# Optimization experiments

Hardware: AMD Instinct MI355X
Metric: run time of the kernel (lower is better)

Reference implementation:

```python
import jax, jax.numpy as jnp
import numpy as np

B, M, C, S, SD, K, H = 32, 448, 384, 512, 128, 8, 8
DH = C // H
EPS = 1e-5
NEG_SLOPE = 0.2


def setup_inputs() -> dict:
    key = jax.random.key(0)
    ks = iter(jax.random.split(key, 32))
    nrm = lambda shape, scale=0.05: (jax.random.normal(next(ks), shape, jnp.float32) * scale)
    inp = {
        'q': jax.random.normal(next(ks), (B, M, C), jnp.float32),
        'coarse': jax.random.normal(next(ks), (B, M, 3), jnp.float32),
        'skeleton': jax.random.normal(next(ks), (B, S, 3), jnp.float32),
        # GraphConv 1: 3 -> 64 (root weight, rel/neighbor weight, bias)
        'gc1_wroot': nrm((3, 64), 0.3), 'gc1_wrel': nrm((3, 64), 0.3), 'gc1_b': jnp.zeros((64,), jnp.float32),
        # GraphConv 2: 64 -> SD
        'gc2_wroot': nrm((64, SD), 0.1), 'gc2_wrel': nrm((64, SD), 0.1), 'gc2_b': jnp.zeros((SD,), jnp.float32),
        # skeleton_projection: SD -> C
        'proj_w': nrm((SD, C), 0.08), 'proj_b': jnp.zeros((C,), jnp.float32),
        # MultiheadAttention (torch layout: in_proj (3C, C), out_proj (C, C))
        'attn_in_w': nrm((3 * C, C), 0.05), 'attn_in_b': jnp.zeros((3 * C,), jnp.float32),
        'attn_out_w': nrm((C, C), 0.05), 'attn_out_b': jnp.zeros((C,), jnp.float32),
        # increase_dim: Conv1d(C,1024,1) + BN(1024) + LeakyReLU + Conv1d(1024,1024,1)
        'inc1_w': nrm((1024, C), 0.05), 'inc1_b': jnp.zeros((1024,), jnp.float32),
        'bn_g': jnp.ones((1024,), jnp.float32), 'bn_b': jnp.zeros((1024,), jnp.float32),
        'bn_m': jnp.zeros((1024,), jnp.float32), 'bn_v': jnp.ones((1024,), jnp.float32),
        'inc2_w': nrm((1024, 1024), 0.03), 'inc2_b': jnp.zeros((1024,), jnp.float32),
        # reduce_map: Linear(C + 1024 + 3, C)
        'red_w': nrm((1024 + C + 3, C), 0.03), 'red_b': jnp.zeros((C,), jnp.float32),
    }
    return inp


def _knn_idx(pts):
    # pts: [B,S,3]; per-batch kNN (self excluded), matching knn_graph(k=K, batch=...)
    d2 = jnp.sum((pts[:, :, None, :] - pts[:, None, :, :]) ** 2, axis=-1)  # [B,S,S]
    d2 = d2 + jnp.eye(S, dtype=pts.dtype)[None] * 1e10                       # mask self
    _, idx = jax.lax.top_k(-d2, K)                                           # [B,S,K]
    return idx


def _graph_conv(x, idx, wroot, wrel, b):
    # GraphConv (PyG, aggr='add'): out_i = x_i Wroot + (sum_{j in N(i)} x_j) Wrel + b
    nb = jax.vmap(lambda f, i: f[i])(x, idx)   # [B,S,K,F]
    agg = nb.sum(axis=2)                       # [B,S,F]
    return x @ wroot + agg @ wrel + b


def reference(q, coarse, skeleton, gc1_wroot, gc1_wrel, gc1_b, gc2_wroot, gc2_wrel, gc2_b,
              proj_w, proj_b, attn_in_w, attn_in_b, attn_out_w, attn_out_b,
              inc1_w, inc1_b, bn_g, bn_b, bn_m, bn_v, inc2_w, inc2_b, red_w, red_b):
    # --- skeleton branch: knn graph + 2-layer GraphConv + max-pool + projection ---
    idx = _knn_idx(skeleton)
    h = _graph_conv(skeleton, idx, gc1_wroot, gc1_wrel, gc1_b)
    h = jax.nn.relu(h)
    h = _graph_conv(h, idx, gc2_wroot, gc2_wrel, gc2_b)        # [B,S,SD]
    proxy = jnp.max(h, axis=1)                                  # [B,SD]
    proxy = proxy @ proj_w + proj_b                             # [B,C]
    kv = jnp.broadcast_to(proxy[:, None, :], (B, M, C))         # expanded proxies

    # --- cross attention (torch nn.MultiheadAttention math) ---
    wq, wk, wv = attn_in_w[:C], attn_in_w[C:2 * C], attn_in_w[2 * C:]
    bq, bk, bv = attn_in_b[:C], attn_in_b[C:2 * C], attn_in_b[2 * C:]
    qh = (q @ wq.T + bq).reshape(B, M, H, DH)
    kh = (kv @ wk.T + bk).reshape(B, M, H, DH)
    vh = (kv @ wv.T + bv).reshape(B, M, H, DH)
    scores = jnp.einsum('bmhd,bnhd->bhmn', qh, kh) / jnp.sqrt(jnp.float32(DH))
    attn = jax.nn.softmax(scores, axis=-1)
    ctx = jnp.einsum('bhmn,bnhd->bmhd', attn, vh).reshape(B, M, C)
    q = ctx @ attn_out_w.T + attn_out_b                         # fused features [B,M,C]

    # --- increase_dim (1x1 conv == matmul) + BN(eval) + LeakyReLU + 1x1 conv ---
    g = jnp.einsum('bmc,oc->bmo', q, inc1_w) + inc1_b           # [B,M,1024]
    g = bn_g * (g - bn_m) * jax.lax.rsqrt(bn_v + EPS) + bn_b
    g = jnp.where(g >= 0, g, NEG_SLOPE * g)
    g = jnp.einsum('bmc,oc->bmo', g, inc2_w) + inc2_b
    global_feature = jnp.max(g, axis=1)                         # [B,1024]

    # --- concat + reduce_map ---
    rebuild = jnp.concatenate([jnp.broadcast_to(global_feature[:, None, :], (B, M, 1024)), q, coarse], axis=-1)
    out = rebuild @ red_w + red_b                               # [B,M,C]
    return out
```

## Files before the change

kernel.cpp:

```cpp
#include <hip/hip_runtime.h>

#define NB 32
#define MM 448
#define CC 384
#define SS 512
#define KNN 8

#define WS_IDX   0u
#define WS_H1    524288u
#define WS_PMAX  (WS_H1 + 4194304u)
#define WS_Q     (WS_PMAX + 262144u)
#define WS_Y     (WS_Q + 49152u)
#define WS_G2    (WS_Y + 131072u)
#define WS_BASEP (WS_G2 + 131072u)
#define WS_PP    WS_H1
#define WS_KV    WS_IDX
#define WS_VV    (WS_IDX + 49152u)

__device__ __forceinline__ float wave_sum(float v) {
#pragma unroll
  for (int m = 1; m < 64; m <<= 1) v += __shfl_xor(v, m, 64);
  return v;
}

__global__ __launch_bounds__(256) void k_knn_gc1(
    const float* __restrict__ skel,
    const float* __restrict__ w1root, const float* __restrict__ w1rel,
    const float* __restrict__ b1,
    int* __restrict__ idx_ws, float* __restrict__ h1_ws)
{
  int b   = blockIdx.x >> 7;
  int grp = blockIdx.x & 127;
  __shared__ __align__(16) float4 sk[SS];
  const float* sb = skel + b * SS * 3;
  for (int t = threadIdx.x; t < SS; t += 256)
    sk[t] = make_float4(sb[t*3+0], sb[t*3+1], sb[t*3+2], 0.f);
  __syncthreads();

  int wave = threadIdx.x >> 6, lane = threadIdx.x & 63;
  int i = grp * 4 + wave;
  float4 pi = sk[i];

  float bd[KNN];
#pragma unroll
  for (int t = 0; t < KNN; t++) {
    int j = lane + (t << 6);
    float4 p = sk[j];
    float d2;
    {
#pragma clang fp contract(off)
      float dx = pi.x - p.x, dy = pi.y - p.y, dz = pi.z - p.z;
      d2 = (dx*dx + dy*dy) + dz*dz;
    }
    bd[t] = (j == i) ? 3e38f : d2;
  }

  int win[KNN];
  int* idx_base = idx_ws + (size_t)(b*SS + i) * KNN;
#pragma unroll
  for (int t = 0; t < KNN; t++) {
    float bestd = bd[0]; int bests = 0;
#pragma unroll
    for (int s = 1; s < KNN; s++)
      if (bd[s] < bestd) { bestd = bd[s]; bests = s; }
    int bestj = lane + (bests << 6);
#pragma unroll
    for (int m = 1; m < 64; m <<= 1) {
      float od = __shfl_xor(bestd, m, 64);
      int   oj = __shfl_xor(bestj, m, 64);
      if (od < bestd || (od == bestd && oj < bestj)) { bestd = od; bestj = oj; }
    }
    win[t] = bestj;
    if (lane == t) idx_base[t] = bestj;
    if ((bestj & 63) == lane) {
      int sl = bestj >> 6;
#pragma unroll
      for (int s = 0; s < KNN; s++) if (s == sl) bd[s] = 3e38f;
    }
  }

  float a0 = 0.f, a1 = 0.f, a2 = 0.f;
#pragma unroll
  for (int t = 0; t < KNN; t++) {
    float4 n = sk[win[t]];
    a0 += n.x; a1 += n.y; a2 += n.z;
  }

  int c = lane;
  float h = b1[c] + pi.x*w1root[c] + pi.y*w1root[64+c] + pi.z*w1root[128+c]
                  + a0*w1rel[c]   + a1*w1rel[64+c]   + a2*w1rel[128+c];
  h = fmaxf(h, 0.f);
  h1_ws[(size_t)(b*SS + i) * 64 + lane] = h;
}

__global__ __launch_bounds__(256) void k_gc2_max(
    const float* __restrict__ h1_ws, const int* __restrict__ idx_ws,
    const float* __restrict__ w2root, const float* __restrict__ w2rel,
    const float* __restrict__ b2, float* __restrict__ pmax)
{
  int b = blockIdx.x >> 4, chunk = blockIdx.x & 15;
  int r0 = chunk * 32;
  __shared__ __align__(16) float X[32*129];
  __shared__ __align__(16) float Wt[32*128];
  __shared__ float mred[8*128];
  __shared__ int nbs[32*KNN];

  const float* h1b = h1_ws + (size_t)b * SS * 64;
  nbs[threadIdx.x] = idx_ws[(b*SS + r0)*KNN + threadIdx.x];
#pragma unroll
  for (int p = 0; p < 8; p++) {
    int idx = threadIdx.x + 256*p;
    int r = idx >> 6, k = idx & 63;
    X[r*129 + k] = h1b[(r0 + r)*64 + k];
  }
  __syncthreads();
#pragma unroll
  for (int p = 0; p < 8; p++) {
    int idx = threadIdx.x + 256*p;
    int r = idx >> 6, k = idx & 63;
    const int* nb = nbs + r*KNN;
    float s = 0.f;
#pragma unroll
    for (int j = 0; j < KNN; j++) s += h1b[nb[j]*64 + k];
    X[r*129 + 64 + k] = s;
  }

  int rg = threadIdx.x >> 5, cg = threadIdx.x & 31;
  float acc[4][4];
#pragma unroll
  for (int r = 0; r < 4; r++)
#pragma unroll
    for (int u = 0; u < 4; u++) acc[r][u] = 0.f;

  const float* wsrc[4] = { w2root, w2root + 32*128, w2rel, w2rel + 32*128 };
#pragma unroll 1
  for (int ch = 0; ch < 4; ch++) {
    __syncthreads();
    const float* ws = wsrc[ch];
#pragma unroll
    for (int p = 0; p < 16; p++) {
      int idx = threadIdx.x + 256*p;
      Wt[idx] = ws[idx];
    }
    __syncthreads();
    int kb = ch * 32;
    const float* xr0 = X + (rg*4+0)*129 + kb;
    const float* xr1 = X + (rg*4+1)*129 + kb;
    const float* xr2 = X + (rg*4+2)*129 + kb;
    const float* xr3 = X + (rg*4+3)*129 + kb;
#pragma unroll 4
    for (int k = 0; k < 32; k++) {
      float4 w4 = *(const float4*)(Wt + k*128 + cg*4);
      float x0 = xr0[k], x1 = xr1[k], x2 = xr2[k], x3 = xr3[k];
      acc[0][0] += x0*w4.x; acc[0][1] += x0*w4.y; acc[0][2] += x0*w4.z; acc[0][3] += x0*w4.w;
      acc[1][0] += x1*w4.x; acc[1][1] += x1*w4.y; acc[1][2] += x1*w4.z; acc[1][3] += x1*w4.w;
      acc[2][0] += x2*w4.x; acc[2][1] += x2*w4.y; acc[2][2] += x2*w4.z; acc[2][3] += x2*w4.w;
      acc[3][0] += x3*w4.x; acc[3][1] += x3*w4.y; acc[3][2] += x3*w4.z; acc[3][3] += x3*w4.w;
    }
  }
#pragma unroll
  for (int u = 0; u < 4; u++)
    mred[rg*128 + cg*4 + u] =
      fmaxf(fmaxf(acc[0][u], acc[1][u]), fmaxf(acc[2][u], acc[3][u]));
  __syncthreads();
  if (threadIdx.x < 128) {
    int col = threadIdx.x;
    float mx = mred[col];
#pragma unroll
    for (int g = 1; g < 8; g++) mx = fmaxf(mx, mred[g*128 + col]);
    pmax[(size_t)(b*16 + chunk)*128 + col] = mx + b2[col];
  }
}

__global__ __launch_bounds__(384) void k_proxy_kv(
    const float* __restrict__ pmax,
    const float* __restrict__ proj_w, const float* __restrict__ proj_b,
    float* __restrict__ kv_ws)
{
  int b = blockIdx.x, t = threadIdx.x;
  __shared__ float proxy[128];
  if (t < 128) {
    float m = -3e38f;
    for (int ch = 0; ch < 16; ch++) m = fmaxf(m, pmax[(size_t)(b*16 + ch)*128 + t]);
    proxy[t] = m;
  }
  __syncthreads();
  float acc = proj_b[t];
  for (int s = 0; s < 128; s++) acc += proxy[s] * proj_w[s*CC + t];
  kv_ws[b*CC + t] = acc;
}

__global__ __launch_bounds__(256) void k_mv384(
    const float* __restrict__ xin, const float* __restrict__ w, int row0,
    const float* __restrict__ bias, int bias0, float* __restrict__ out)
{
  int b = blockIdx.x, og = blockIdx.y;
  int wv = threadIdx.x >> 6, lane = threadIdx.x & 63;
  __shared__ float xs[CC];
  for (int t = threadIdx.x; t < CC; t += 256) xs[t] = xin[b*CC + t];
  __syncthreads();
  float x0 = xs[lane*6+0], x1 = xs[lane*6+1], x2 = xs[lane*6+2];
  float x3 = xs[lane*6+3], x4 = xs[lane*6+4], x5 = xs[lane*6+5];
#pragma unroll
  for (int u = 0; u < 8; u++) {
    int o = og*32 + wv*8 + u;
    const float* wr = w + (size_t)(row0 + o) * CC + lane*6;
    float2 wa = *(const float2*)wr;
    float2 wb = *(const float2*)(wr + 2);
    float2 wc = *(const float2*)(wr + 4);
    float p = wa.x*x0 + wa.y*x1 + wb.x*x2 + wb.y*x3 + wc.x*x4 + wc.y*x5;
    p = wave_sum(p);
    if (lane == 0) out[b*CC + o] = bias[bias0 + o] + p;
  }
}

__global__ __launch_bounds__(256) void k_inc1_bn(
    const float* __restrict__ q_ws, const float* __restrict__ inc1_w,
    const float* __restrict__ inc1_b,
    const float* __restrict__ bng, const float* __restrict__ bnb,
    const float* __restrict__ bnm, const float* __restrict__ bnv,
    float* __restrict__ y_ws)
{
  int b = blockIdx.x >> 4, og = blockIdx.x & 15;
  int t = threadIdx.x;
  int o = og*64 + (t >> 2), qq = t & 3;
  __shared__ __align__(16) float xs[CC];
  for (int i = t; i < CC; i += 256) xs[i] = q_ws[b*CC + i];
  __syncthreads();
  const float* wr = inc1_w + (size_t)o * CC + qq*96;
  const float* xr = xs + qq*96;
  float acc = 0.f;
#pragma unroll
  for (int kk = 0; kk < 96; kk += 4) {
    float4 w4 = *(const float4*)(wr + kk);
    float4 x4 = *(const float4*)(xr + kk);
    acc += w4.x*x4.x + w4.y*x4.y + w4.z*x4.z + w4.w*x4.w;
  }
  acc += __shfl_xor(acc, 1, 64);
  acc += __shfl_xor(acc, 2, 64);
  if (qq == 0) {
    float a = acc + inc1_b[o];
    float z = bng[o] * (a - bnm[o]) * rsqrtf(bnv[o] + 1e-5f) + bnb[o];
    y_ws[b*1024 + o] = (z >= 0.f) ? z : 0.2f * z;
  }
}

__global__ __launch_bounds__(256) void k_inc2(
    const float* __restrict__ y_ws, const float* __restrict__ inc2_w,
    const float* __restrict__ inc2_b, float* __restrict__ g2_ws)
{
  int b = blockIdx.x >> 4, og = blockIdx.x & 15;
  int t = threadIdx.x;
  int o = og*64 + (t >> 2), qq = t & 3;
  __shared__ __align__(16) float xs[1024];
  for (int i = t; i < 1024; i += 256) xs[i] = y_ws[b*1024 + i];
  __syncthreads();
  const float* wr = inc2_w + (size_t)o * 1024 + qq*256;
  const float* xr = xs + qq*256;
  float acc = 0.f;
#pragma unroll 8
  for (int kk = 0; kk < 256; kk += 4) {
    float4 w4 = *(const float4*)(wr + kk);
    float4 x4 = *(const float4*)(xr + kk);
    acc += w4.x*x4.x + w4.y*x4.y + w4.z*x4.z + w4.w*x4.w;
  }
  acc += __shfl_xor(acc, 1, 64);
  acc += __shfl_xor(acc, 2, 64);
  if (qq == 0) g2_ws[b*1024 + o] = acc + inc2_b[o];
}

__global__ __launch_bounds__(256) void k_basep(
    const float* __restrict__ g2_ws, const float* __restrict__ q_ws,
    const float* __restrict__ red_w, float* __restrict__ pp)
{
  int cg = blockIdx.x;
  int o0 = blockIdx.y * 64;
  int c0 = cg * 32;
  __shared__ __align__(16) float xs[32*33];
  __shared__ __align__(16) float wt[32*64];
#pragma unroll
  for (int p = 0; p < 8; p++) {
    int idx = threadIdx.x + 256*p;
    int c = idx >> 6, o = idx & 63;
    wt[idx] = red_w[(size_t)(c0 + c)*CC + o0 + o];
  }
  {
    int b = threadIdx.x >> 3, cp = threadIdx.x & 7;
    const float* src = (cg < 32) ? (g2_ws + b*1024 + c0)
                                 : (q_ws  + b*CC   + (c0 - 1024));
    float4 v = *(const float4*)(src + cp*4);
    xs[(cp*4+0)*33 + b] = v.x;
    xs[(cp*4+1)*33 + b] = v.y;
    xs[(cp*4+2)*33 + b] = v.z;
    xs[(cp*4+3)*33 + b] = v.w;
  }
  __syncthreads();
  int b = threadIdx.x >> 3, og = threadIdx.x & 7;
  float acc[8];
#pragma unroll
  for (int u = 0; u < 8; u++) acc[u] = 0.f;
#pragma unroll 8
  for (int c = 0; c < 32; c++) {
    float xv = xs[c*33 + b];
    float4 w0 = *(const float4*)(wt + c*64 + og*8);
    float4 w1 = *(const float4*)(wt + c*64 + og*8 + 4);
    acc[0] += xv*w0.x; acc[1] += xv*w0.y; acc[2] += xv*w0.z; acc[3] += xv*w0.w;
    acc[4] += xv*w1.x; acc[5] += xv*w1.y; acc[6] += xv*w1.z; acc[7] += xv*w1.w;
  }
  float* dst = pp + (size_t)(cg*32 + b)*CC + o0 + og*8;
  *(float4*)dst       = make_float4(acc[0], acc[1], acc[2], acc[3]);
  *(float4*)(dst + 4) = make_float4(acc[4], acc[5], acc[6], acc[7]);
}

__global__ __launch_bounds__(256) void k_base_red(
    const float* __restrict__ pp, float* __restrict__ basep)
{
  int idx = blockIdx.x * 256 + threadIdx.x;
  float s = 0.f;
#pragma unroll 4
  for (int cg = 0; cg < 44; cg++) s += pp[cg*12288 + idx];
  basep[idx] = s;
}

__global__ __launch_bounds__(256) void k_out(
    const float* __restrict__ basep, const float* __restrict__ red_b,
    const float* __restrict__ red_w, const float* __restrict__ coarse,
    float* __restrict__ out)
{
  int gid = blockIdx.x * 256 + threadIdx.x;
  int c4 = gid % 96;
  int row = gid / 96;
  int b = row / 448;
  int c = c4 * 4;
  float4 p0 = *(const float4*)(basep + b*CC + c);
  float4 rb = *(const float4*)(red_b + c);
  const float* cr = coarse + (size_t)row * 3;
  float cx = cr[0], cy = cr[1], cz = cr[2];
  float4 w0 = *(const float4*)(red_w + (size_t)1408*CC + c);
  float4 w1 = *(const float4*)(red_w + (size_t)1409*CC + c);
  float4 w2 = *(const float4*)(red_w + (size_t)1410*CC + c);
  float4 o4;
  o4.x = p0.x + rb.x + cx*w0.x + cy*w1.x + cz*w2.x;
  o4.y = p0.y + rb.y + cx*w0.y + cy*w1.y + cz*w2.y;
  o4.z = p0.z + rb.z + cx*w0.z + cy*w1.z + cz*w2.z;
  o4.w = p0.w + rb.w + cx*w0.w + cy*w1.w + cz*w2.w;
  *(float4*)(out + (size_t)row*CC + c) = o4;
}

extern "C" void kernel_launch(void* const* d_in, const int* in_sizes, int n_in,
                              void* d_out, int out_size, void* d_ws, size_t ws_size,
                              hipStream_t stream)
{
  (void)in_sizes; (void)n_in; (void)out_size; (void)ws_size;
  const float* coarse = (const float*)d_in[1];
  const float* skel   = (const float*)d_in[2];
  const float* g1wr   = (const float*)d_in[3];
  const float* g1wl   = (const float*)d_in[4];
  const float* g1b    = (const float*)d_in[5];
  const float* g2wr   = (const float*)d_in[6];
  const float* g2wl   = (const float*)d_in[7];
  const float* g2b    = (const float*)d_in[8];
  const float* projw  = (const float*)d_in[9];
  const float* projb  = (const float*)d_in[10];
  const float* aiw    = (const float*)d_in[11];
  const float* aib    = (const float*)d_in[12];
  const float* aow    = (const float*)d_in[13];
  const float* aob    = (const float*)d_in[14];
  const float* i1w    = (const float*)d_in[15];
  const float* i1b    = (const float*)d_in[16];
  const float* bng    = (const float*)d_in[17];
  const float* bnb    = (const float*)d_in[18];
  const float* bnm    = (const float*)d_in[19];
  const float* bnv    = (const float*)d_in[20];
  const float* i2w    = (const float*)d_in[21];
  const float* i2b    = (const float*)d_in[22];
  const float* redw   = (const float*)d_in[23];
  const float* redb   = (const float*)d_in[24];
  float* out = (float*)d_out;

  char* ws = (char*)d_ws;
  int*   idx_ws = (int*)(ws + WS_IDX);
  float* h1_ws  = (float*)(ws + WS_H1);
  float* pmax   = (float*)(ws + WS_PMAX);
  float* q_ws   = (float*)(ws + WS_Q);
  float* y_ws   = (float*)(ws + WS_Y);
  float* g2_ws  = (float*)(ws + WS_G2);
  float* basep  = (float*)(ws + WS_BASEP);
  float* pp     = (float*)(ws + WS_PP);
  float* kv_ws  = (float*)(ws + WS_KV);
  float* vv_ws  = (float*)(ws + WS_VV);

  k_knn_gc1<<<4096, 256, 0, stream>>>(skel, g1wr, g1wl, g1b, idx_ws, h1_ws);
  k_gc2_max<<<512, 256, 0, stream>>>(h1_ws, idx_ws, g2wr, g2wl, g2b, pmax);
  k_proxy_kv<<<32, 384, 0, stream>>>(pmax, projw, projb, kv_ws);
  k_mv384<<<dim3(32, 12), 256, 0, stream>>>(kv_ws, aiw, 2*CC, aib, 2*CC, vv_ws);
  k_mv384<<<dim3(32, 12), 256, 0, stream>>>(vv_ws, aow, 0,    aob, 0,    q_ws);
  k_inc1_bn<<<512, 256, 0, stream>>>(q_ws, i1w, i1b, bng, bnb, bnm, bnv, y_ws);
  k_inc2<<<512, 256, 0, stream>>>(y_ws, i2w, i2b, g2_ws);
  k_basep<<<dim3(44, 6), 256, 0, stream>>>(g2_ws, q_ws, redw, pp);
  k_base_red<<<48, 256, 0, stream>>>(pp, basep);
  k_out<<<5376, 256, 0, stream>>>(basep, redb, redw, coarse, out);
}
```

Measured before the change: 234.2 us.

## Fuse all stages into one cooperative persistent kernel with grid syncs

Replaces the ten separate kernel launches with a single cooperative kernel of 512 blocks that runs every stage in turn, separated by grid-wide barriers. Stages that used more blocks now loop over virtual blocks, and smaller stages idle the extra blocks. The goal is to remove per-launch overhead and inter-kernel gaps. In exchange it adds grid.sync costs, lower parallelism for the large kNN and output stages, and a dependence on all 512 blocks being co-resident.

```diff
diff --git a/kernel.cpp b/kernel.cpp
--- a/kernel.cpp
+++ b/kernel.cpp
@@ -1,10 +1,14 @@
 #include <hip/hip_runtime.h>
+#include <hip/hip_cooperative_groups.h>
+
+namespace cg = cooperative_groups;
 
 #define NB 32
 #define MM 448
 #define CC 384
 #define SS 512
 #define KNN 8
+#define NBLK 512
 
 #define WS_IDX   0u
 #define WS_H1    524288u
@@ -17,334 +21,340 @@
 #define WS_KV    WS_IDX
 #define WS_VV    (WS_IDX + 49152u)
 
+struct P {
+  const float *coarse, *skel, *g1wr, *g1wl, *g1b, *g2wr, *g2wl, *g2b,
+              *projw, *projb, *aiw, *aib, *aow, *aob, *i1w, *i1b,
+              *bng, *bnb, *bnm, *bnv, *i2w, *i2b, *redw, *redb;
+  int* idx_ws;
+  float *h1_ws, *pmax, *q_ws, *y_ws, *g2_ws, *basep, *pp, *kv_ws, *vv_ws, *out;
+};
+
 __device__ __forceinline__ float wave_sum(float v) {
 #pragma unroll
   for (int m = 1; m < 64; m <<= 1) v += __shfl_xor(v, m, 64);
   return v;
 }
 
-__global__ __launch_bounds__(256) void k_knn_gc1(
-    const float* __restrict__ skel,
-    const float* __restrict__ w1root, const float* __restrict__ w1rel,
-    const float* __restrict__ b1,
-    int* __restrict__ idx_ws, float* __restrict__ h1_ws)
-{
-  int b   = blockIdx.x >> 7;
-  int grp = blockIdx.x & 127;
-  __shared__ __align__(16) float4 sk[SS];
-  const float* sb = skel + b * SS * 3;
-  for (int t = threadIdx.x; t < SS; t += 256)
-    sk[t] = make_float4(sb[t*3+0], sb[t*3+1], sb[t*3+2], 0.f);
-  __syncthreads();
-
-  int wave = threadIdx.x >> 6, lane = threadIdx.x & 63;
-  int i = grp * 4 + wave;
-  float4 pi = sk[i];
-
-  float bd[KNN];
-#pragma unroll
-  for (int t = 0; t < KNN; t++) {
-    int j = lane + (t << 6);
-    float4 p = sk[j];
-    float d2;
+__global__ __launch_bounds__(256, 2) void k_all(P p) {
+  cg::grid_group grid = cg::this_grid();
+  __shared__ __align__(16) float smem[9600];
+  const int tid = threadIdx.x;
+  const int bid = blockIdx.x;
+
+  {
+    float4* sk = (float4*)smem;
+    for (int vb = bid; vb < 4096; vb += NBLK) {
+      int b = vb >> 7, grp = vb & 127;
+      __syncthreads();
+      const float* sb = p.skel + b * SS * 3;
+      for (int t = tid; t < SS; t += 256)
+        sk[t] = make_float4(sb[t*3+0], sb[t*3+1], sb[t*3+2], 0.f);
+      __syncthreads();
+
+      int wave = tid >> 6, lane = tid & 63;
+      int i = grp * 4 + wave;
+      float4 pi = sk[i];
+      float bd[KNN];
+#pragma unroll
+      for (int t = 0; t < KNN; t++) {
+        int j = lane + (t << 6);
+        float4 q = sk[j];
+        float d2;
+        {
+#pragma clang fp contract(off)
+          float dx = pi.x - q.x, dy = pi.y - q.y, dz = pi.z - q.z;
+          d2 = (dx*dx + dy*dy) + dz*dz;
+        }
+        bd[t] = (j == i) ? 3e38f : d2;
+      }
+      int win[KNN];
+      int* idx_base = p.idx_ws + (size_t)(b*SS + i) * KNN;
+#pragma unroll
+      for (int t = 0; t < KNN; t++) {
+        float bestd = bd[0]; int bests = 0;
+#pragma unroll
+        for (int s = 1; s < KNN; s++)
+          if (bd[s] < bestd) { bestd = bd[s]; bests = s; }
+        int bestj = lane + (bests << 6);
+#pragma unroll
+        for (int m = 1; m < 64; m <<= 1) {
+          float od = __shfl_xor(bestd, m, 64);
+          int   oj = __shfl_xor(bestj, m, 64);
+          if (od < bestd || (od == bestd && oj < bestj)) { bestd = od; bestj = oj; }
+        }
+        win[t] = bestj;
+        if (lane == t) idx_base[t] = bestj;
+        if ((bestj & 63) == lane) {
+          int sl = bestj >> 6;
+#pragma unroll
+          for (int s = 0; s < KNN; s++) if (s == sl) bd[s] = 3e38f;
+        }
+      }
+      float a0 = 0.f, a1 = 0.f, a2 = 0.f;
+#pragma unroll
+      for (int t = 0; t < KNN; t++) {
+        float4 n = sk[win[t]];
+        a0 += n.x; a1 += n.y; a2 += n.z;
+      }
+      int c = lane;
+      float h = p.g1b[c] + pi.x*p.g1wr[c] + pi.y*p.g1wr[64+c] + pi.z*p.g1wr[128+c]
+                         + a0*p.g1wl[c]   + a1*p.g1wl[64+c]   + a2*p.g1wl[128+c];
+      p.h1_ws[(size_t)(b*SS + i) * 64 + lane] = fmaxf(h, 0.f);
+    }
+  }
+  grid.sync();
+
+  {
+    float* X    = smem;
+    float* Wt   = smem + 4128;
+    float* mred = smem + 8224;
+    int*   nbs  = (int*)(smem + 9248);
+    int b = bid >> 4, chunk = bid & 15;
+    int r0 = chunk * 32;
+    const float* h1b = p.h1_ws + (size_t)b * SS * 64;
+    nbs[tid] = p.idx_ws[(b*SS + r0)*KNN + tid];
+#pragma unroll
+    for (int q = 0; q < 8; q++) {
+      int idx = tid + 256*q;
+      int r = idx >> 6, k = idx & 63;
+      X[r*129 + k] = h1b[(r0 + r)*64 + k];
+    }
+    __syncthreads();
+#pragma unroll
+    for (int q = 0; q < 8; q++) {
+      int idx = tid + 256*q;
+      int r = idx >> 6, k = idx & 63;
+      const int* nb = nbs + r*KNN;
+      float s = 0.f;
+#pragma unroll
+      for (int j = 0; j < KNN; j++) s += h1b[nb[j]*64 + k];
+      X[r*129 + 64 + k] = s;
+    }
+    int rg = tid >> 5, cgi = tid & 31;
+    float acc[4][4];
+#pragma unroll
+    for (int r = 0; r < 4; r++)
+#pragma unroll
+      for (int u = 0; u < 4; u++) acc[r][u] = 0.f;
+    const float* wsrc[4] = { p.g2wr, p.g2wr + 32*128, p.g2wl, p.g2wl + 32*128 };
+#pragma unroll 1
+    for (int ch = 0; ch < 4; ch++) {
+      __syncthreads();
+      const float* ws = wsrc[ch];
+#pragma unroll
+      for (int q = 0; q < 16; q++) {
+        int idx = tid + 256*q;
+        Wt[idx] = ws[idx];
+      }
+      __syncthreads();
+      int kb = ch * 32;
+      const float* xr0 = X + (rg*4+0)*129 + kb;
+      const float* xr1 = X + (rg*4+1)*129 + kb;
+      const float* xr2 = X + (rg*4+2)*129 + kb;
+      const float* xr3 = X + (rg*4+3)*129 + kb;
+#pragma unroll 4
+      for (int k = 0; k < 32; k++) {
+        float4 w4 = *(const float4*)(Wt + k*128 + cgi*4);
+        float x0 = xr0[k], x1 = xr1[k], x2 = xr2[k], x3 = xr3[k];
+        acc[0][0] += x0*w4.x; acc[0][1] += x0*w4.y; acc[0][2] += x0*w4.z; acc[0][3] += x0*w4.w;
+        acc[1][0] += x1*w4.x; acc[1][1] += x1*w4.y; acc[1][2] += x1*w4.z; acc[1][3] += x1*w4.w;
+        acc[2][0] += x2*w4.x; acc[2][1] += x2*w4.y; acc[2][2] += x2*w4.z; acc[2][3] += x2*w4.w;
+        acc[3][0] += x3*w4.x; acc[3][1] += x3*w4.y; acc[3][2] += x3*w4.z; acc[3][3] += x3*w4.w;
+      }
+    }
+#pragma unroll
+    for (int u = 0; u < 4; u++)
+      mred[rg*128 + cgi*4 + u] =
+        fmaxf(fmaxf(acc[0][u], acc[1][u]), fmaxf(acc[2][u], acc[3][u]));
+    __syncthreads();
+    if (tid < 128) {
+      int col = tid;
+      float mx = mred[col];
+#pragma unroll
+      for (int g = 1; g < 8; g++) mx = fmaxf(mx, mred[g*128 + col]);
+      p.pmax[(size_t)(b*16 + chunk)*128 + col] = mx + p.g2b[col];
+    }
+  }
+  grid.sync();
+
+  if (bid < NB) {
+    float* proxy = smem;
+    int b = bid;
+    if (tid < 128) {
+      float m = -3e38f;
+      for (int ch = 0; ch < 16; ch++)
+        m = fmaxf(m, p.pmax[(size_t)(b*16 + ch)*128 + tid]);
+      proxy[tid] = m;
+    }
+    __syncthreads();
+    for (int c = tid; c < CC; c += 256) {
+      float acc = p.projb[c];
+      for (int s = 0; s < 128; s++) acc += proxy[s] * p.projw[s*CC + c];
+      p.kv_ws[b*CC + c] = acc;
+    }
+  }
+  grid.sync();
+
+  if (bid < 384) {
+    float* xs = smem;
+    int b = bid & 31, og = bid >> 5;
+    int wv = tid >> 6, lane = tid & 63;
+    for (int t = tid; t < CC; t += 256) xs[t] = p.kv_ws[b*CC + t];
+    __syncthreads();
+    float x0 = xs[lane*6+0], x1 = xs[lane*6+1], x2 = xs[lane*6+2];
+    float x3 = xs[lane*6+3], x4 = xs[lane*6+4], x5 = xs[lane*6+5];
+#pragma unroll
+    for (int u = 0; u < 8; u++) {
+      int o = og*32 + wv*8 + u;
+      const float* wr = p.aiw + (size_t)(2*CC + o) * CC + lane*6;
+      float2 wa = *(const float2*)wr;
+      float2 wb = *(const float2*)(wr + 2);
+      float2 wc = *(const float2*)(wr + 4);
+      float pr = wa.x*x0 + wa.y*x1 + wb.x*x2 + wb.y*x3 + wc.x*x4 + wc.y*x5;
+      pr = wave_sum(pr);
+      if (lane == 0) p.vv_ws[b*CC + o] = p.aib[2*CC + o] + pr;
+    }
+  }
+  grid.sync();
+
+  if (bid < 384) {
+    float* xs = smem;
+    int b = bid & 31, og = bid >> 5;
+    int wv = tid >> 6, lane = tid & 63;
+    for (int t = tid; t < CC; t += 256) xs[t] = p.vv_ws[b*CC + t];
+    __syncthreads();
+    float x0 = xs[lane*6+0], x1 = xs[lane*6+1], x2 = xs[lane*6+2];
+    float x3 = xs[lane*6+3], x4 = xs[lane*6+4], x5 = xs[lane*6+5];
+#pragma unroll
+    for (int u = 0; u < 8; u++) {
+      int o = og*32 + wv*8 + u;
+      const float* wr = p.aow + (size_t)o * CC + lane*6;
+      float2 wa = *(const float2*)wr;
+      float2 wb = *(const float2*)(wr + 2);
+      float2 wc = *(const float2*)(wr + 4);
+      float pr = wa.x*x0 + wa.y*x1 + wb.x*x2 + wb.y*x3 + wc.x*x4 + wc.y*x5;
+      pr = wave_sum(pr);
+      if (lane == 0) p.q_ws[b*CC + o] = p.aob[o] + pr;
+    }
+  }
+  grid.sync();
+
+  {
+    float* xs = smem;
+    int b = bid >> 4, og = bid & 15;
+    int o = og*64 + (tid >> 2), qq = tid & 3;
+    for (int i = tid; i < CC; i += 256) xs[i] = p.q_ws[b*CC + i];
+    __syncthreads();
+    const float* wr = p.i1w + (size_t)o * CC + qq*96;
+    const float* xr = xs + qq*96;
+    float acc = 0.f;
+#pragma unroll
+    for (int kk = 0; kk < 96; kk += 4) {
+      float4 w4 = *(const float4*)(wr + kk);
+      float4 x4 = *(const float4*)(xr + kk);
+      acc += w4.x*x4.x + w4.y*x4.y + w4.z*x4.z + w4.w*x4.w;
+    }
+    acc += __shfl_xor(acc, 1, 64);
+    acc += __shfl_xor(acc, 2, 64);
+    if (qq == 0) {
+      float a = acc + p.i1b[o];
+      float z = p.bng[o] * (a - p.bnm[o]) * rsqrtf(p.bnv[o] + 1e-5f) + p.bnb[o];
+      p.y_ws[b*1024 + o] = (z >= 0.f) ? z : 0.2f * z;
+    }
+  }
+  grid.sync();
+
+  {
+    float* xs = smem;
+    int b = bid >> 4, og = bid & 15;
+    int o = og*64 + (tid >> 2), qq = tid & 3;
+    for (int i = tid; i < 1024; i += 256) xs[i] = p.y_ws[b*1024 + i];
+    __syncthreads();
+    const float* wr = p.i2w + (size_t)o * 1024 + qq*256;
+    const float* xr = xs + qq*256;
+    float acc = 0.f;
+#pragma unroll 8
+    for (int kk = 0; kk < 256; kk += 4) {
+      float4 w4 = *(const float4*)(wr + kk);
+      float4 x4 = *(const float4*)(xr + kk);
+      acc += w4.x*x4.x + w4.y*x4.y + w4.z*x4.z + w4.w*x4.w;
+    }
+    acc += __shfl_xor(acc, 1, 64);
+    acc += __shfl_xor(acc, 2, 64);
+    if (qq == 0) p.g2_ws[b*1024 + o] = acc + p.i2b[o];
+  }
+  grid.sync();
+
+  if (bid < 264) {
+    float* xs = smem;
+    float* wt = smem + 1056;
+    int cg = bid % 44, o0 = (bid / 44) * 64;
+    int c0 = cg * 32;
+#pragma unroll
+    for (int q = 0; q < 8; q++) {
+      int idx = tid + 256*q;
+      int c = idx >> 6, o = idx & 63;
+      wt[idx] = p.redw[(size_t)(c0 + c)*CC + o0 + o];
+    }
     {
-#pragma clang fp contract(off)
-      float dx = pi.x - p.x, dy = pi.y - p.y, dz = pi.z - p.z;
-      d2 = (dx*dx + dy*dy) + dz*dz;
-    }
-    bd[t] = (j == i) ? 3e38f : d2;
-  }
-
-  int win[KNN];
-  int* idx_base = idx_ws + (size_t)(b*SS + i) * KNN;
-#pragma unroll
-  for (int t = 0; t < KNN; t++) {
-    float bestd = bd[0]; int bests = 0;
-#pragma unroll
-    for (int s = 1; s < KNN; s++)
-      if (bd[s] < bestd) { bestd = bd[s]; bests = s; }
-    int bestj = lane + (bests << 6);
-#pragma unroll
-    for (int m = 1; m < 64; m <<= 1) {
-      float od = __shfl_xor(bestd, m, 64);
-      int   oj = __shfl_xor(bestj, m, 64);
-      if (od < bestd || (od == bestd && oj < bestj)) { bestd = od; bestj = oj; }
-    }
-    win[t] = bestj;
-    if (lane == t) idx_base[t] = bestj;
-    if ((bestj & 63) == lane) {
-      int sl = bestj >> 6;
-#pragma unroll
-      for (int s = 0; s < KNN; s++) if (s == sl) bd[s] = 3e38f;
-    }
-  }
-
-  float a0 = 0.f, a1 = 0.f, a2 = 0.f;
-#pragma unroll
-  for (int t = 0; t < KNN; t++) {
-    float4 n = sk[win[t]];
-    a0 += n.x; a1 += n.y; a2 += n.z;
-  }
-
-  int c = lane;
-  float h = b1[c] + pi.x*w1root[c] + pi.y*w1root[64+c] + pi.z*w1root[128+c]
-                  + a0*w1rel[c]   + a1*w1rel[64+c]   + a2*w1rel[128+c];
-  h = fmaxf(h, 0.f);
-  h1_ws[(size_t)(b*SS + i) * 64 + lane] = h;
-}
-
-__global__ __launch_bounds__(256) void k_gc2_max(
-    const float* __restrict__ h1_ws, const int* __restrict__ idx_ws,
-    const float* __restrict__ w2root, const float* __restrict__ w2rel,
-    const float* __restrict__ b2, float* __restrict__ pmax)
-{
-  int b = blockIdx.x >> 4, chunk = blockIdx.x & 15;
-  int r0 = chunk * 32;
-  __shared__ __align__(16) float X[32*129];
-  __shared__ __align__(16) float Wt[32*128];
-  __shared__ float mred[8*128];
-  __shared__ int nbs[32*KNN];
-
-  const float* h1b = h1_ws + (size_t)b * SS * 64;
-  nbs[threadIdx.x] = idx_ws[(b*SS + r0)*KNN + threadIdx.x];
-#pragma unroll
-  for (int p = 0; p < 8; p++) {
-    int idx = threadIdx.x + 256*p;
-    int r = idx >> 6, k = idx & 63;
-    X[r*129 + k] = h1b[(r0 + r)*64 + k];
-  }
-  __syncthreads();
-#pragma unroll
-  for (int p = 0; p < 8; p++) {
-    int idx = threadIdx.x + 256*p;
-    int r = idx >> 6, k = idx & 63;
-    const int* nb = nbs + r*KNN;
+      int b = tid >> 3, cp = tid & 7;
+      const float* src = (cg < 32) ? (p.g2_ws + b*1024 + c0)
+                                   : (p.q_ws  + b*CC   + (c0 - 1024));
+      float4 v = *(const float4*)(src + cp*4);
+      xs[(cp*4+0)*33 + b] = v.x;
+      xs[(cp*4+1)*33 + b] = v.y;
+      xs[(cp*4+2)*33 + b] = v.z;
+      xs[(cp*4+3)*33 + b] = v.w;
+    }
+    __syncthreads();
+    int b = tid >> 3, og = tid & 7;
+    float acc[8];
+#pragma unroll
+    for (int u = 0; u < 8; u++) acc[u] = 0.f;
+#pragma unroll 8
+    for (int c = 0; c < 32; c++) {
+      float xv = xs[c*33 + b];
+      float4 w0 = *(const float4*)(wt + c*64 + og*8);
+      float4 w1 = *(const float4*)(wt + c*64 + og*8 + 4);
+      acc[0] += xv*w0.x; acc[1] += xv*w0.y; acc[2] += xv*w0.z; acc[3] += xv*w0.w;
+      acc[4] += xv*w1.x; acc[5] += xv*w1.y; acc[6] += xv*w1.z; acc[7] += xv*w1.w;
+    }
+    float* dst = p.pp + (size_t)(cg*32 + b)*CC + o0 + og*8;
+    *(float4*)dst       = make_float4(acc[0], acc[1], acc[2], acc[3]);
+    *(float4*)(dst + 4) = make_float4(acc[4], acc[5], acc[6], acc[7]);
+  }
+  grid.sync();
+
+  if (bid < 48) {
+    int idx = bid * 256 + tid;
     float s = 0.f;
-#pragma unroll
-    for (int j = 0; j < KNN; j++) s += h1b[nb[j]*64 + k];
-    X[r*129 + 64 + k] = s;
-  }
-
-  int rg = threadIdx.x >> 5, cg = threadIdx.x & 31;
-  float acc[4][4];
-#pragma unroll
-  for (int r = 0; r < 4; r++)
-#pragma unroll
-    for (int u = 0; u < 4; u++) acc[r][u] = 0.f;
-
-  const float* wsrc[4] = { w2root, w2root + 32*128, w2rel, w2rel + 32*128 };
-#pragma unroll 1
-  for (int ch = 0; ch < 4; ch++) {
-    __syncthreads();
-    const float* ws = wsrc[ch];
-#pragma unroll
-    for (int p = 0; p < 16; p++) {
-      int idx = threadIdx.x + 256*p;
-      Wt[idx] = ws[idx];
-    }
-    __syncthreads();
-    int kb = ch * 32;
-    const float* xr0 = X + (rg*4+0)*129 + kb;
-    const float* xr1 = X + (rg*4+1)*129 + kb;
-    const float* xr2 = X + (rg*4+2)*129 + kb;
-    const float* xr3 = X + (rg*4+3)*129 + kb;
 #pragma unroll 4
-    for (int k = 0; k < 32; k++) {
-      float4 w4 = *(const float4*)(Wt + k*128 + cg*4);
-      float x0 = xr0[k], x1 = xr1[k], x2 = xr2[k], x3 = xr3[k];
-      acc[0][0] += x0*w4.x; acc[0][1] += x0*w4.y; acc[0][2] += x0*w4.z; acc[0][3] += x0*w4.w;
-      acc[1][0] += x1*w4.x; acc[1][1] += x1*w4.y; acc[1][2] += x1*w4.z; acc[1][3] += x1*w4.w;
-      acc[2][0] += x2*w4.x; acc[2][1] += x2*w4.y; acc[2][2] += x2*w4.z; acc[2][3] += x2*w4.w;
-      acc[3][0] += x3*w4.x; acc[3][1] += x3*w4.y; acc[3][2] += x3*w4.z; acc[3][3] += x3*w4.w;
-    }
-  }
-#pragma unroll
-  for (int u = 0; u < 4; u++)
-    mred[rg*128 + cg*4 + u] =
-      fmaxf(fmaxf(acc[0][u], acc[1][u]), fmaxf(acc[2][u], acc[3][u]));
-  __syncthreads();
-  if (threadIdx.x < 128) {
-    int col = threadIdx.x;
-    float mx = mred[col];
-#pragma unroll
-    for (int g = 1; g < 8; g++) mx = fmaxf(mx, mred[g*128 + col]);
-    pmax[(size_t)(b*16 + chunk)*128 + col] = mx + b2[col];
-  }
-}
-
-__global__ __launch_bounds__(384) void k_proxy_kv(
-    const float* __restrict__ pmax,
-    const float* __restrict__ proj_w, const float* __restrict__ proj_b,
-    float* __restrict__ kv_ws)
-{
-  int b = blockIdx.x, t = threadIdx.x;
-  __shared__ float proxy[128];
-  if (t < 128) {
-    float m = -3e38f;
-    for (int ch = 0; ch < 16; ch++) m = fmaxf(m, pmax[(size_t)(b*16 + ch)*128 + t]);
-    proxy[t] = m;
-  }
-  __syncthreads();
-  float acc = proj_b[t];
-  for (int s = 0; s < 128; s++) acc += proxy[s] * proj_w[s*CC + t];
-  kv_ws[b*CC + t] = acc;
-}
-
-__global__ __launch_bounds__(256) void k_mv384(
-    const float* __restrict__ xin, const float* __restrict__ w, int row0,
-    const float* __restrict__ bias, int bias0, float* __restrict__ out)
-{
-  int b = blockIdx.x, og = blockIdx.y;
-  int wv = threadIdx.x >> 6, lane = threadIdx.x & 63;
-  __shared__ float xs[CC];
-  for (int t = threadIdx.x; t < CC; t += 256) xs[t] = xin[b*CC + t];
-  __syncthreads();
-  float x0 = xs[lane*6+0], x1 = xs[lane*6+1], x2 = xs[lane*6+2];
-  float x3 = xs[lane*6+3], x4 = xs[lane*6+4], x5 = xs[lane*6+5];
-#pragma unroll
-  for (int u = 0; u < 8; u++) {
-    int o = og*32 + wv*8 + u;
-    const float* wr = w + (size_t)(row0 + o) * CC + lane*6;
-    float2 wa = *(const float2*)wr;
-    float2 wb = *(const float2*)(wr + 2);
-    float2 wc = *(const float2*)(wr + 4);
-    float p = wa.x*x0 + wa.y*x1 + wb.x*x2 + wb.y*x3 + wc.x*x4 + wc.y*x5;
-    p = wave_sum(p);
-    if (lane == 0) out[b*CC + o] = bias[bias0 + o] + p;
-  }
-}
-
-__global__ __launch_bounds__(256) void k_inc1_bn(
-    const float* __restrict__ q_ws, const float* __restrict__ inc1_w,
-    const float* __restrict__ inc1_b,
-    const float* __restrict__ bng, const float* __restrict__ bnb,
-    const float* __restrict__ bnm, const float* __restrict__ bnv,
-    float* __restrict__ y_ws)
-{
-  int b = blockIdx.x >> 4, og = blockIdx.x & 15;
-  int t = threadIdx.x;
-  int o = og*64 + (t >> 2), qq = t & 3;
-  __shared__ __align__(16) float xs[CC];
-  for (int i = t; i < CC; i += 256) xs[i] = q_ws[b*CC + i];
-  __syncthreads();
-  const float* wr = inc1_w + (size_t)o * CC + qq*96;
-  const float* xr = xs + qq*96;
-  float acc = 0.f;
-#pragma unroll
-  for (int kk = 0; kk < 96; kk += 4) {
-    float4 w4 = *(const float4*)(wr + kk);
-    float4 x4 = *(const float4*)(xr + kk);
-    acc += w4.x*x4.x + w4.y*x4.y + w4.z*x4.z + w4.w*x4.w;
-  }
-  acc += __shfl_xor(acc, 1, 64);
-  acc += __shfl_xor(acc, 2, 64);
-  if (qq == 0) {
-    float a = acc + inc1_b[o];
-    float z = bng[o] * (a - bnm[o]) * rsqrtf(bnv[o] + 1e-5f) + bnb[o];
-    y_ws[b*1024 + o] = (z >= 0.f) ? z : 0.2f * z;
-  }
-}
-
-__global__ __launch_bounds__(256) void k_inc2(
-    const float* __restrict__ y_ws, const float* __restrict__ inc2_w,
-    const float* __restrict__ inc2_b, float* __restrict__ g2_ws)
-{
-  int b = blockIdx.x >> 4, og = blockIdx.x & 15;
-  int t = threadIdx.x;
-  int o = og*64 + (t >> 2), qq = t & 3;
-  __shared__ __align__(16) float xs[1024];
-  for (int i = t; i < 1024; i += 256) xs[i] = y_ws[b*1024 + i];
-  __syncthreads();
-  const float* wr = inc2_w + (size_t)o * 1024 + qq*256;
-  const float* xr = xs + qq*256;
-  float acc = 0.f;
-#pragma unroll 8
-  for (int kk = 0; kk < 256; kk += 4) {
-    float4 w4 = *(const float4*)(wr + kk);
-    float4 x4 = *(const float4*)(xr + kk);
-    acc += w4.x*x4.x + w4.y*x4.y + w4.z*x4.z + w4.w*x4.w;
-  }
-  acc += __shfl_xor(acc, 1, 64);
-  acc += __shfl_xor(acc, 2, 64);
-  if (qq == 0) g2_ws[b*1024 + o] = acc + inc2_b[o];
-}
-
-__global__ __launch_bounds__(256) void k_basep(
-    const float* __restrict__ g2_ws, const float* __restrict__ q_ws,
-    const float* __restrict__ red_w, float* __restrict__ pp)
-{
-  int cg = blockIdx.x;
-  int o0 = blockIdx.y * 64;
-  int c0 = cg * 32;
-  __shared__ __align__(16) float xs[32*33];
-  __shared__ __align__(16) float wt[32*64];
-#pragma unroll
-  for (int p = 0; p < 8; p++) {
-    int idx = threadIdx.x + 256*p;
-    int c = idx >> 6, o = idx & 63;
-    wt[idx] = red_w[(size_t)(c0 + c)*CC + o0 + o];
-  }
+    for (int cg = 0; cg < 44; cg++) s += p.pp[cg*12288 + idx];
+    p.basep[idx] = s;
+  }
+  grid.sync();
+
   {
-    int b = threadIdx.x >> 3, cp = threadIdx.x & 7;
-    const float* src = (cg < 32) ? (g2_ws + b*1024 + c0)
-                                 : (q_ws  + b*CC   + (c0 - 1024));
-    float4 v = *(const float4*)(src + cp*4);
-    xs[(cp*4+0)*33 + b] = v.x;
-    xs[(cp*4+1)*33 + b] = v.y;
-    xs[(cp*4+2)*33 + b] = v.z;
-    xs[(cp*4+3)*33 + b] = v.w;
-  }
-  __syncthreads();
-  int b = threadIdx.x >> 3, og = threadIdx.x & 7;
-  float acc[8];
-#pragma unroll
-  for (int u = 0; u < 8; u++) acc[u] = 0.f;
-#pragma unroll 8
-  for (int c = 0; c < 32; c++) {
-    float xv = xs[c*33 + b];
-    float4 w0 = *(const float4*)(wt + c*64 + og*8);
-    float4 w1 = *(const float4*)(wt + c*64 + og*8 + 4);
-    acc[0] += xv*w0.x; acc[1] += xv*w0.y; acc[2] += xv*w0.z; acc[3] += xv*w0.w;
-    acc[4] += xv*w1.x; acc[5] += xv*w1.y; acc[6] += xv*w1.z; acc[7] += xv*w1.w;
-  }
-  float* dst = pp + (size_t)(cg*32 + b)*CC + o0 + og*8;
-  *(float4*)dst       = make_float4(acc[0], acc[1], acc[2], acc[3]);
-  *(float4*)(dst + 4) = make_float4(acc[4], acc[5], acc[6], acc[7]);
-}
-
-__global__ __launch_bounds__(256) void k_base_red(
-    const float* __restrict__ pp, float* __restrict__ basep)
-{
-  int idx = blockIdx.x * 256 + threadIdx.x;
-  float s = 0.f;
-#pragma unroll 4
-  for (int cg = 0; cg < 44; cg++) s += pp[cg*12288 + idx];
-  basep[idx] = s;
-}
-
-__global__ __launch_bounds__(256) void k_out(
-    const float* __restrict__ basep, const float* __restrict__ red_b,
-    const float* __restrict__ red_w, const float* __restrict__ coarse,
-    float* __restrict__ out)
-{
-  int gid = blockIdx.x * 256 + threadIdx.x;
-  int c4 = gid % 96;
-  int row = gid / 96;
-  int b = row / 448;
-  int c = c4 * 4;
-  float4 p0 = *(const float4*)(basep + b*CC + c);
-  float4 rb = *(const float4*)(red_b + c);
-  const float* cr = coarse + (size_t)row * 3;
-  float cx = cr[0], cy = cr[1], cz = cr[2];
-  float4 w0 = *(const float4*)(red_w + (size_t)1408*CC + c);
-  float4 w1 = *(const float4*)(red_w + (size_t)1409*CC + c);
-  float4 w2 = *(const float4*)(red_w + (size_t)1410*CC + c);
-  float4 o4;
-  o4.x = p0.x + rb.x + cx*w0.x + cy*w1.x + cz*w2.x;
-  o4.y = p0.y + rb.y + cx*w0.y + cy*w1.y + cz*w2.y;
-  o4.z = p0.z + rb.z + cx*w0.z + cy*w1.z + cz*w2.z;
-  o4.w = p0.w + rb.w + cx*w0.w + cy*w1.w + cz*w2.w;
-  *(float4*)(out + (size_t)row*CC + c) = o4;
+    for (int gid = bid * 256 + tid; gid < 32*448*96; gid += NBLK*256) {
+      int c4 = gid % 96;
+      int row = gid / 96;
+      int b = row / 448;
+      int c = c4 * 4;
+      float4 p0 = *(const float4*)(p.basep + b*CC + c);
+      float4 rb = *(const float4*)(p.redb + c);
+      const float* cr = p.coarse + (size_t)row * 3;
+      float cx = cr[0], cy = cr[1], cz = cr[2];
+      float4 w0 = *(const float4*)(p.redw + (size_t)1408*CC + c);
+      float4 w1 = *(const float4*)(p.redw + (size_t)1409*CC + c);
+      float4 w2 = *(const float4*)(p.redw + (size_t)1410*CC + c);
+      float4 o4;
+      o4.x = p0.x + rb.x + cx*w0.x + cy*w1.x + cz*w2.x;
+      o4.y = p0.y + rb.y + cx*w0.y + cy*w1.y + cz*w2.y;
+      o4.z = p0.z + rb.z + cx*w0.z + cy*w1.z + cz*w2.z;
+      o4.w = p0.w + rb.w + cx*w0.w + cy*w1.w + cz*w2.w;
+      *(float4*)(p.out + (size_t)row*CC + c) = o4;
+    }
+  }
 }
 
 extern "C" void kernel_launch(void* const* d_in, const int* in_sizes, int n_in,
@@ -352,52 +362,45 @@
                               hipStream_t stream)
 {
   (void)in_sizes; (void)n_in; (void)out_size; (void)ws_size;
-  const float* coarse = (const float*)d_in[1];
-  const float* skel   = (const float*)d_in[2];
-  const float* g1wr   = (const float*)d_in[3];
-  const float* g1wl   = (const float*)d_in[4];
-  const float* g1b    = (const float*)d_in[5];
-  const float* g2wr   = (const float*)d_in[6];
-  const float* g2wl   = (const float*)d_in[7];
-  const float* g2b    = (const float*)d_in[8];
-  const float* projw  = (const float*)d_in[9];
-  const float* projb  = (const float*)d_in[10];
-  const float* aiw    = (const float*)d_in[11];
-  const float* aib    = (const float*)d_in[12];
-  const float* aow    = (const float*)d_in[13];
-  const float* aob    = (const float*)d_in[14];
-  const float* i1w    = (const float*)d_in[15];
-  const float* i1b    = (const float*)d_in[16];
-  const float* bng    = (const float*)d_in[17];
-  const float* bnb    = (const float*)d_in[18];
-  const float* bnm    = (const float*)d_in[19];
-  const float* bnv    = (const float*)d_in[20];
-  const float* i2w    = (const float*)d_in[21];
-  const float* i2b    = (const float*)d_in[22];
-  const float* redw   = (const float*)d_in[23];
-  const float* redb   = (const float*)d_in[24];
-  float* out = (float*)d_out;
-
   char* ws = (char*)d_ws;
-  int*   idx_ws = (int*)(ws + WS_IDX);
-  float* h1_ws  = (float*)(ws + WS_H1);
-  float* pmax   = (float*)(ws + WS_PMAX);
-  float* q_ws   = (float*)(ws + WS_Q);
-  float* y_ws   = (float*)(ws + WS_Y);
-  float* g2_ws  = (float*)(ws + WS_G2);
-  float* basep  = (float*)(ws + WS_BASEP);
-  float* pp     = (float*)(ws + WS_PP);
-  float* kv_ws  = (float*)(ws + WS_KV);
-  float* vv_ws  = (float*)(ws + WS_VV);
-
-  k_knn_gc1<<<4096, 256, 0, stream>>>(skel, g1wr, g1wl, g1b, idx_ws, h1_ws);
-  k_gc2_max<<<512, 256, 0, stream>>>(h1_ws, idx_ws, g2wr, g2wl, g2b, pmax);
-  k_proxy_kv<<<32, 384, 0, stream>>>(pmax, projw, projb, kv_ws);
-  k_mv384<<<dim3(32, 12), 256, 0, stream>>>(kv_ws, aiw, 2*CC, aib, 2*CC, vv_ws);
-  k_mv384<<<dim3(32, 12), 256, 0, stream>>>(vv_ws, aow, 0,    aob, 0,    q_ws);
-  k_inc1_bn<<<512, 256, 0, stream>>>(q_ws, i1w, i1b, bng, bnb, bnm, bnv, y_ws);
-  k_inc2<<<512, 256, 0, stream>>>(y_ws, i2w, i2b, g2_ws);
-  k_basep<<<dim3(44, 6), 256, 0, stream>>>(g2_ws, q_ws, redw, pp);
-  k_base_red<<<48, 256, 0, stream>>>(pp, basep);
-  k_out<<<5376, 256, 0, stream>>>(basep, redb, redw, coarse, out);
+  P prm;
+  prm.coarse = (const float*)d_in[1];
+  prm.skel   = (const float*)d_in[2];
+  prm.g1wr   = (const float*)d_in[3];
+  prm.g1wl   = (const float*)d_in[4];
+  prm.g1b    = (const float*)d_in[5];
+  prm.g2wr   = (const float*)d_in[6];
+  prm.g2wl   = (const float*)d_in[7];
+  prm.g2b    = (const float*)d_in[8];
+  prm.projw  = (const float*)d_in[9];
+  prm.projb  = (const float*)d_in[10];
+  prm.aiw    = (const float*)d_in[11];
+  prm.aib    = (const float*)d_in[12];
+  prm.aow    = (const float*)d_in[13];
+  prm.aob    = (const float*)d_in[14];
+  prm.i1w    = (const float*)d_in[15];
+  prm.i1b    = (const float*)d_in[16];
+  prm.bng    = (const float*)d_in[17];
+  prm.bnb    = (const float*)d_in[18];
+  prm.bnm    = (const float*)d_in[19];
+  prm.bnv    = (const float*)d_in[20];
+  prm.i2w    = (const float*)d_in[21];
+  prm.i2b    = (const float*)d_in[22];
+  prm.redw   = (const float*)d_in[23];
+  prm.redb   = (const float*)d_in[24];
+  prm.idx_ws = (int*)(ws + WS_IDX);
+  prm.h1_ws  = (float*)(ws + WS_H1);
+  prm.pmax   = (float*)(ws + WS_PMAX);
+  prm.q_ws   = (float*)(ws + WS_Q);
+  prm.y_ws   = (float*)(ws + WS_Y);
+  prm.g2_ws  = (float*)(ws + WS_G2);
+  prm.basep  = (float*)(ws + WS_BASEP);
+  prm.pp     = (float*)(ws + WS_PP);
+  prm.kv_ws  = (float*)(ws + WS_KV);
+  prm.vv_ws  = (float*)(ws + WS_VV);
+  prm.out    = (float*)d_out;
+
+  void* args[] = { &prm };
+  hipLaunchCooperativeKernel((const void*)k_all, dim3(NBLK), dim3(256),
+                             args, 0, stream);
 }
```

Measured after the change: 750.0 us. 3.2x slower.
